# Optimization experiments

Measured on AMD Instinct MI355X. Metric: run time of the kernel, lower is better.

Reference implementation:

```python
import jax, jax.numpy as jnp
import numpy as np

N_NODES = 100000
N_EDGES = 1600000
IN_DIM, HID_DIM, OUT_DIM = 128, 64, 64


def setup_inputs() -> dict:
    key = jax.random.key(0)
    ks = jax.random.split(key, 8)
    x = jax.random.normal(ks[0], (N_NODES, IN_DIM), dtype=jnp.float32)
    edge_index = jax.random.randint(ks[1], (2, N_EDGES), 0, N_NODES, dtype=jnp.int32)
    edge_weight = jax.random.uniform(ks[2], (N_EDGES,), dtype=jnp.float32)
    # GCNConv parameters (glorot-ish init)
    w1 = jax.random.normal(ks[3], (IN_DIM, HID_DIM), dtype=jnp.float32) / np.sqrt(IN_DIM)
    b1 = jnp.zeros((HID_DIM,), dtype=jnp.float32)
    w2 = jax.random.normal(ks[4], (HID_DIM, OUT_DIM), dtype=jnp.float32) / np.sqrt(HID_DIM)
    b2 = jnp.zeros((OUT_DIM,), dtype=jnp.float32)
    return {"x": x, "edge_index": edge_index, "edge_weight": edge_weight,
            "w1": w1, "b1": b1, "w2": w2, "b2": b2}


def _gcn_conv(h, src, dst, edge_weight, w, b, n_nodes):
    # GCNConv(normalize=False): linear transform, then edge-weighted scatter-add
    # (source_to_target flow: gather from src, scatter-sum into dst), then bias.
    h = h @ w                                   # [N, out]
    msg = h[src] * edge_weight[:, None]          # [E, out] irregular gather
    agg = jax.ops.segment_sum(msg, dst, num_segments=n_nodes)  # [N, out]
    return agg + b


def reference(x, edge_index, edge_weight, w1, b1, w2, b2):
    src, dst = edge_index[0], edge_index[1]
    n = x.shape[0]
    # Dropout is identity in eval mode (training=False).
    h = _gcn_conv(x, src, dst, edge_weight, w1, b1, n)
    h = jax.nn.relu(h)
    out = _gcn_conv(h, src, dst, edge_weight, w2, b2, n)
    return out
```

## Files before the change

kernel.cpp:

```cpp
#include <hip/hip_runtime.h>
#include <hip/hip_bf16.h>


#define N_NODES 100000
#define N_EDGES 1600000
#define NB1     391
#define T1      4096
#define NT1     391
#define CAP1    4706
#define GB1     782

typedef unsigned short ushort_t;
typedef unsigned int uint_t;
typedef __attribute__((ext_vector_type(8))) short bf16x8;
typedef __attribute__((ext_vector_type(4))) float floatx4;
typedef __attribute__((ext_vector_type(8))) ushort_t ushort8v;

static __device__ __forceinline__ float bf2f(ushort_t h) {
    return __uint_as_float(((uint_t)h) << 16);
}
static __device__ __forceinline__ ushort_t f2bf(float f) {
    uint_t u = __float_as_uint(f);
    u = (u + 0x7FFF + ((u >> 16) & 1)) >> 16;
    return (ushort_t)u;
}

__global__ __launch_bounds__(512) void k_init(int* __restrict__ gcursor)
{
    int t = threadIdx.x;
    if (t < NB1) gcursor[t] = t * CAP1;
}

__global__ __launch_bounds__(512) void k_p1g1(
    const int* __restrict__ src, const int* __restrict__ dst,
    const float* __restrict__ ew, int* __restrict__ gcursor,
    int2* __restrict__ recs1, int E,
    const float* __restrict__ X, const float* __restrict__ W,
    ushort_t* __restrict__ Y, int N)
{
    __shared__ __align__(16) char smem[47296];
    const int tid = threadIdx.x;

    if (blockIdx.x < NT1) {
        int* cnt     = (int*)smem;
        int* start   = cnt + NB1;
        int* cursor  = start + NB1;
        int* gb      = cursor + NB1;
        int* wsum    = (int*)(smem + 6256);
        int* wexc    = wsum + 8;
        int2* stg    = (int2*)(smem + 6336);
        ushort_t* sb = (ushort_t*)(smem + 39104);
        const int t = tid, b = blockIdx.x;
        const int lane = t & 63, wv = t >> 6;

        if (t < NB1) cnt[t] = 0;
        __syncthreads();
        const int e0 = b * T1;
        const int e1 = min(E, e0 + T1);
        for (int e = e0 + t; e < e1; e += 512)
            atomicAdd(&cnt[dst[e] >> 8], 1);
        __syncthreads();

        const int v = (t < NB1) ? cnt[t] : 0;
        int x = v;
        #pragma unroll
        for (int off = 1; off < 64; off <<= 1) {
            int y = __shfl_up(x, off);
            if (lane >= off) x += y;
        }
        if (lane == 63) wsum[wv] = x;
        __syncthreads();
        if (t < 8) {
            int w  = wsum[t];
            int xx = w;
            #pragma unroll
            for (int off = 1; off < 8; off <<= 1) {
                int y = __shfl_up(xx, off);
                if (t >= off) xx += y;
            }
            wexc[t] = xx - w;
        }
        __syncthreads();
        if (t < NB1) {
            int st = x + wexc[wv] - v;
            start[t]  = st;
            cursor[t] = st;
            gb[t]     = atomicAdd(&gcursor[t], v);
        }
        __syncthreads();

        for (int e = e0 + t; e < e1; e += 512) {
            int d  = dst[e];
            int bk = d >> 8;
            int p  = atomicAdd(&cursor[bk], 1);
            int2 r;
            r.x = ((d & 255) << 17) | src[e];
            r.y = __float_as_int(ew[e]);
            stg[p] = r;
            sb[p]  = (ushort_t)bk;
        }
        __syncthreads();
        const int n = e1 - e0;
        for (int i = t; i < n; i += 512) {
            int bk = sb[i];
            recs1[gb[bk] + (i - start[bk])] = stg[i];
        }
    } else {
        ushort_t* sA = (ushort_t*)smem;
        ushort_t* sB = (ushort_t*)(smem + 18432);
        const int b    = blockIdx.x - NT1;
        const int row0 = b * 128;

        for (int i = tid; i < 128 * 16; i += 512) {
            int k = i >> 4, n4 = (i & 15) * 4;
            float4 v = *(const float4*)(W + (size_t)k * 64 + n4);
            sB[(n4 + 0) * 136 + k] = f2bf(v.x);
            sB[(n4 + 1) * 136 + k] = f2bf(v.y);
            sB[(n4 + 2) * 136 + k] = f2bf(v.z);
            sB[(n4 + 3) * 136 + k] = f2bf(v.w);
        }
        for (int i = tid; i < 128 * 16; i += 512) {
            int r = i >> 4, c4 = (i & 15) * 4;
            int rg = row0 + r; if (rg > N - 1) rg = N - 1;
            float4 v = *(const float4*)(X + (size_t)rg * 128 + c4);
            *(ushort4*)(sA + r * 72 + c4) =
                make_ushort4(f2bf(v.x), f2bf(v.y), f2bf(v.z), f2bf(v.w));
        }
        __syncthreads();

        const int wid = tid >> 6, lane = tid & 63;
        const int m = lane & 15, quad = lane >> 4;
        floatx4 acc[4] = {};

        #pragma unroll
        for (int ksl = 0; ksl < 2; ++ksl) {
            bf16x8 a = *(const bf16x8*)(sA + (wid * 16 + m) * 72 + ksl * 32 + quad * 8);
            #pragma unroll
            for (int nt = 0; nt < 4; ++nt) {
                bf16x8 bfr = *(const bf16x8*)(sB + (nt * 16 + m) * 136 + ksl * 32 + quad * 8);
                acc[nt] = __builtin_amdgcn_mfma_f32_16x16x32_bf16(a, bfr, acc[nt], 0, 0, 0);
            }
        }
        __syncthreads();
        for (int i = tid; i < 128 * 16; i += 512) {
            int r = i >> 4, c4 = (i & 15) * 4;
            int rg = row0 + r; if (rg > N - 1) rg = N - 1;
            float4 v = *(const float4*)(X + (size_t)rg * 128 + 64 + c4);
            *(ushort4*)(sA + r * 72 + c4) =
                make_ushort4(f2bf(v.x), f2bf(v.y), f2bf(v.z), f2bf(v.w));
        }
        __syncthreads();
        #pragma unroll
        for (int ksl = 0; ksl < 2; ++ksl) {
            bf16x8 a = *(const bf16x8*)(sA + (wid * 16 + m) * 72 + ksl * 32 + quad * 8);
            #pragma unroll
            for (int nt = 0; nt < 4; ++nt) {
                bf16x8 bfr = *(const bf16x8*)(sB + (nt * 16 + m) * 136 + 64 + ksl * 32 + quad * 8);
                acc[nt] = __builtin_amdgcn_mfma_f32_16x16x32_bf16(a, bfr, acc[nt], 0, 0, 0);
            }
        }
        __syncthreads();
        #pragma unroll
        for (int nt = 0; nt < 4; ++nt)
            #pragma unroll
            for (int r = 0; r < 4; ++r)
                sA[(wid * 16 + quad * 4 + r) * 72 + nt * 16 + m] = f2bf(acc[nt][r]);
        __syncthreads();
        for (int i = tid; i < 128 * 8; i += 512) {
            int rr = i >> 3, c8 = (i & 7) * 8;
            int rg = row0 + rr;
            if (rg < N)
                *(ushort8v*)(Y + (size_t)rg * 64 + c8) =
                    *(const ushort8v*)(sA + rr * 72 + c8);
        }
    }
}

__global__ __launch_bounds__(1024) void k_pass2(
    const int2* __restrict__ recs1, const int* __restrict__ gcursor,
    int2* __restrict__ recs2, int2* __restrict__ nodeinfo, int N)
{
    __shared__ int cnt[256];
    __shared__ int s[256];
    __shared__ int cursor[256];
    const int t = threadIdx.x, b = blockIdx.x;
    const int lo = b * CAP1;
    const int hi = gcursor[b];

    if (t < 256) cnt[t] = 0;
    __syncthreads();
    for (int j = lo + t; j < hi; j += 1024)
        atomicAdd(&cnt[((uint_t)recs1[j].x) >> 17], 1);
    __syncthreads();
    const int v = (t < 256) ? cnt[t] : 0;
    if (t < 256) s[t] = v;
    #pragma unroll
    for (int off = 1; off < 256; off <<= 1) {
        __syncthreads();
        int a = (t >= off && t < 256) ? s[t - off] : 0;
        __syncthreads();
        if (t < 256) s[t] += a;
    }
    __syncthreads();
    if (t < 256) {
        const int stl = s[t] - v;
        cursor[t] = stl;
        const int ng = b * 256 + t;
        if (ng < N) {
            int2 ni; ni.x = lo + stl; ni.y = v;
            nodeinfo[ng] = ni;
        }
    }
    __syncthreads();
    for (int j = lo + t; j < hi; j += 1024) {
        int2 r = recs1[j];
        int dl = ((uint_t)r.x) >> 17;
        int p  = atomicAdd(&cursor[dl], 1);
        int2 o;
        o.x = r.x & 0x1FFFF;
        o.y = r.y;
        recs2[lo + p] = o;
    }
}

__global__ __launch_bounds__(256) void k_gather1(
    const ushort_t* __restrict__ H, const int2* __restrict__ recs,
    const int2* __restrict__ nodeinfo, const float* __restrict__ bias,
    ushort_t* __restrict__ out)
{
    const int wid  = threadIdx.x >> 6;
    const int lane = threadIdx.x & 63;
    const int n0   = (blockIdx.x * 4 + wid) * 2;
    const int n1   = n0 + 1;

    const int2 niA = nodeinfo[n0];
    const int2 niB = nodeinfo[n1];
    int baseA = niA.x; const int endA = niA.x + niA.y;
    int baseB = niB.x; const int endB = niB.x + niB.y;

    const int g  = lane >> 4;
    const int c4 = (lane & 15) * 4;

    float a0 = 0.f, a1 = 0.f, a2 = 0.f, a3 = 0.f;
    float b0 = 0.f, b1 = 0.f, b2 = 0.f, b3 = 0.f;

    while (baseA < endA || baseB < endB) {
        int mA = endA - baseA; if (mA > 64) mA = 64;
        int mB = endB - baseB; if (mB > 64) mB = 64;
        int2 rA = (mA > 0) ? recs[baseA + (lane < mA ? lane : mA - 1)]
                           : make_int2(0, 0);
        int2 rB = (mB > 0) ? recs[baseB + (lane < mB ? lane : mB - 1)]
                           : make_int2(0, 0);
        float wAf = __int_as_float(rA.y);
        float wBf = __int_as_float(rB.y);
        int mm = mA > mB ? mA : mB;
        #pragma unroll 4
        for (int jj = 0; jj < mm; jj += 4) {
            int idx = jj + g;
            int   sA = __shfl(rA.x, idx);
            float wA = __shfl(wAf, idx);
            int   sB = __shfl(rB.x, idx);
            float wB = __shfl(wBf, idx);
            if (idx >= mA) wA = 0.f;
            if (idx >= mB) wB = 0.f;
            ushort4 hA = *(const ushort4*)(H + (size_t)sA * 64 + c4);
            ushort4 hB = *(const ushort4*)(H + (size_t)sB * 64 + c4);
            a0 = fmaf(wA, bf2f(hA.x), a0);
            a1 = fmaf(wA, bf2f(hA.y), a1);
            a2 = fmaf(wA, bf2f(hA.z), a2);
            a3 = fmaf(wA, bf2f(hA.w), a3);
            b0 = fmaf(wB, bf2f(hB.x), b0);
            b1 = fmaf(wB, bf2f(hB.y), b1);
            b2 = fmaf(wB, bf2f(hB.z), b2);
            b3 = fmaf(wB, bf2f(hB.w), b3);
        }
        baseA += 64;
        baseB += 64;
    }
    a0 += __shfl_down(a0, 32); a1 += __shfl_down(a1, 32);
    a2 += __shfl_down(a2, 32); a3 += __shfl_down(a3, 32);
    b0 += __shfl_down(b0, 32); b1 += __shfl_down(b1, 32);
    b2 += __shfl_down(b2, 32); b3 += __shfl_down(b3, 32);
    a0 += __shfl_down(a0, 16); a1 += __shfl_down(a1, 16);
    a2 += __shfl_down(a2, 16); a3 += __shfl_down(a3, 16);
    b0 += __shfl_down(b0, 16); b1 += __shfl_down(b1, 16);
    b2 += __shfl_down(b2, 16); b3 += __shfl_down(b3, 16);

    if (lane < 16) {
        float4 bv = *(const float4*)(bias + c4);
        float vA0 = fmaxf(a0 + bv.x, 0.f), vA1 = fmaxf(a1 + bv.y, 0.f);
        float vA2 = fmaxf(a2 + bv.z, 0.f), vA3 = fmaxf(a3 + bv.w, 0.f);
        float vB0 = fmaxf(b0 + bv.x, 0.f), vB1 = fmaxf(b1 + bv.y, 0.f);
        float vB2 = fmaxf(b2 + bv.z, 0.f), vB3 = fmaxf(b3 + bv.w, 0.f);
        *(ushort4*)(out + (size_t)n0 * 64 + c4) =
            make_ushort4(f2bf(vA0), f2bf(vA1), f2bf(vA2), f2bf(vA3));
        *(ushort4*)(out + (size_t)n1 * 64 + c4) =
            make_ushort4(f2bf(vB0), f2bf(vB1), f2bf(vB2), f2bf(vB3));
    }
}

__global__ __launch_bounds__(256) void k_gather2mm(
    const ushort_t* __restrict__ H, const int2* __restrict__ recs,
    const int2* __restrict__ nodeinfo, const float* __restrict__ bias2,
    const float* __restrict__ W2, float* __restrict__ out)
{
    __shared__ ushort_t sW[64 * 72];
    __shared__ ushort_t strip[4][128];

    const int tid  = threadIdx.x;
    const int wid  = tid >> 6;
    const int lane = tid & 63;
    const int n0   = (blockIdx.x * 4 + wid) * 2;
    const int n1   = n0 + 1;

    for (int i = tid; i < 64 * 16; i += 256) {
        int k = i >> 4, n4 = (i & 15) * 4;
        float4 v = *(const float4*)(W2 + (size_t)k * 64 + n4);
        sW[(n4 + 0) * 72 + k] = f2bf(v.x);
        sW[(n4 + 1) * 72 + k] = f2bf(v.y);
        sW[(n4 + 2) * 72 + k] = f2bf(v.z);
        sW[(n4 + 3) * 72 + k] = f2bf(v.w);
    }
    __syncthreads();

    const int2 niA = nodeinfo[n0];
    const int2 niB = nodeinfo[n1];
    int baseA = niA.x; const int endA = niA.x + niA.y;
    int baseB = niB.x; const int endB = niB.x + niB.y;

    const int g  = lane >> 4;
    const int c4 = (lane & 15) * 4;

    float a0 = 0.f, a1 = 0.f, a2 = 0.f, a3 = 0.f;
    float b0 = 0.f, b1 = 0.f, b2 = 0.f, b3 = 0.f;

    while (baseA < endA || baseB < endB) {
        int mA = endA - baseA; if (mA > 64) mA = 64;
        int mB = endB - baseB; if (mB > 64) mB = 64;
        int2 rA = (mA > 0) ? recs[baseA + (lane < mA ? lane : mA - 1)]
                           : make_int2(0, 0);
        int2 rB = (mB > 0) ? recs[baseB + (lane < mB ? lane : mB - 1)]
                           : make_int2(0, 0);
        float wAf = __int_as_float(rA.y);
        float wBf = __int_as_float(rB.y);
        int mm = mA > mB ? mA : mB;
        #pragma unroll 4
        for (int jj = 0; jj < mm; jj += 4) {
            int idx = jj + g;
            int   sA_ = __shfl(rA.x, idx);
            float wA  = __shfl(wAf, idx);
            int   sB_ = __shfl(rB.x, idx);
            float wB  = __shfl(wBf, idx);
            if (idx >= mA) wA = 0.f;
            if (idx >= mB) wB = 0.f;
            ushort4 hA = *(const ushort4*)(H + (size_t)sA_ * 64 + c4);
            ushort4 hB = *(const ushort4*)(H + (size_t)sB_ * 64 + c4);
            a0 = fmaf(wA, bf2f(hA.x), a0);
            a1 = fmaf(wA, bf2f(hA.y), a1);
            a2 = fmaf(wA, bf2f(hA.z), a2);
            a3 = fmaf(wA, bf2f(hA.w), a3);
            b0 = fmaf(wB, bf2f(hB.x), b0);
            b1 = fmaf(wB, bf2f(hB.y), b1);
            b2 = fmaf(wB, bf2f(hB.z), b2);
            b3 = fmaf(wB, bf2f(hB.w), b3);
        }
        baseA += 64;
        baseB += 64;
    }
    a0 += __shfl_down(a0, 32); a1 += __shfl_down(a1, 32);
    a2 += __shfl_down(a2, 32); a3 += __shfl_down(a3, 32);
    b0 += __shfl_down(b0, 32); b1 += __shfl_down(b1, 32);
    b2 += __shfl_down(b2, 32); b3 += __shfl_down(b3, 32);
    a0 += __shfl_down(a0, 16); a1 += __shfl_down(a1, 16);
    a2 += __shfl_down(a2, 16); a3 += __shfl_down(a3, 16);
    b0 += __shfl_down(b0, 16); b1 += __shfl_down(b1, 16);
    b2 += __shfl_down(b2, 16); b3 += __shfl_down(b3, 16);

    if (lane < 16) {
        *(ushort4*)(&strip[wid][0 * 64 + c4]) =
            make_ushort4(f2bf(a0), f2bf(a1), f2bf(a2), f2bf(a3));
        *(ushort4*)(&strip[wid][1 * 64 + c4]) =
            make_ushort4(f2bf(b0), f2bf(b1), f2bf(b2), f2bf(b3));
    }
    __builtin_amdgcn_wave_barrier();

    const int m = lane & 15, quad = lane >> 4;
    const ushort_t* sp = strip[wid];
    floatx4 acc2[4] = {};
    #pragma unroll
    for (int ks = 0; ks < 2; ++ks) {
        bf16x8 a = *(const bf16x8*)(sp + (m & 1) * 64 + ks * 32 + quad * 8);
        #pragma unroll
        for (int nt = 0; nt < 4; ++nt) {
            bf16x8 bfr = *(const bf16x8*)(sW + (nt * 16 + m) * 72 + ks * 32 + quad * 8);
            acc2[nt] = __builtin_amdgcn_mfma_f32_16x16x32_bf16(a, bfr, acc2[nt], 0, 0, 0);
        }
    }
    if (quad == 0) {
        #pragma unroll
        for (int nt = 0; nt < 4; ++nt) {
            float bb0 = bias2[nt * 16 + m];
            out[(size_t)n0 * 64 + nt * 16 + m] = acc2[nt][0] + bb0;
            out[(size_t)n1 * 64 + nt * 16 + m] = acc2[nt][1] + bb0;
        }
    }
}

extern "C" void kernel_launch(void* const* d_in, const int* in_sizes, int n_in,
                              void* d_out, int out_size, void* d_ws, size_t ws_size,
                              hipStream_t stream) {
    const float* x   = (const float*)d_in[0];
    const int*   ei  = (const int*)  d_in[1];
    const float* ew  = (const float*)d_in[2];
    const float* w1  = (const float*)d_in[3];
    const float* b1  = (const float*)d_in[4];
    const float* w2  = (const float*)d_in[5];
    const float* b2  = (const float*)d_in[6];
    float* out = (float*)d_out;

    const int N = N_NODES, E = N_EDGES;
    const int* src = ei;
    const int* dst = ei + E;

    char* p = (char*)d_ws;
    ushort_t* bufA   = (ushort_t*)p;  p += (size_t)N_NODES * 64 * 2;
    int2*     recs2  = (int2*)p;      p += (size_t)NB1 * CAP1 * 8;
    int2*     recs1  = (int2*)p;
    ushort_t* bufB   = (ushort_t*)p;  p += (size_t)NB1 * CAP1 * 8;
    int*      gcur   = (int*)p;       p += 2048;
    int2*     ninfo  = (int2*)p;      p += (size_t)N_NODES * 8;

    k_init <<<1, 512, 0, stream>>>(gcur);
    k_p1g1 <<<NT1 + GB1, 512, 0, stream>>>(src, dst, ew, gcur, recs1, E,
                                           x, w1, bufA, N);
    k_pass2<<<NB1, 1024, 0, stream>>>(recs1, gcur, recs2, ninfo, N);

    k_gather1<<<N / 8, 256, 0, stream>>>(bufA, recs2, ninfo, b1, bufB);

    k_gather2mm<<<N / 8, 256, 0, stream>>>(bufB, recs2, ninfo, b2, w2, out);
}
```

Measured before the change: 245.3 us.

## Load full X tile once, simplify block scan, vectorize output stores

The GEMM branch now stages the whole 128x128 X tile in shared memory at once and runs a single 4-step K loop, instead of two half-K passes separated by barriers. The warp-shuffle two-level prefix scan becomes a shared-memory Hillis-Steele scan with many block barriers. The final output stores of the second gather kernel go through a small shared strip so each lane writes a float4 rather than scalar floats. Shared memory per block grows, which may reduce occupancy, and the new scan adds barrier overhead.

```diff
diff --git a/kernel.cpp b/kernel.cpp
--- a/kernel.cpp
+++ b/kernel.cpp
@@ -38,7 +38,7 @@
     const float* __restrict__ X, const float* __restrict__ W,
     ushort_t* __restrict__ Y, int N)
 {
-    __shared__ __align__(16) char smem[47296];
+    __shared__ __align__(16) char smem[52224];
     const int tid = threadIdx.x;
 
     if (blockIdx.x < NT1) {
@@ -46,12 +46,10 @@
         int* start   = cnt + NB1;
         int* cursor  = start + NB1;
         int* gb      = cursor + NB1;
-        int* wsum    = (int*)(smem + 6256);
-        int* wexc    = wsum + 8;
-        int2* stg    = (int2*)(smem + 6336);
-        ushort_t* sb = (ushort_t*)(smem + 39104);
+        int* s       = (int*)(smem + 6256);
+        int2* stg    = (int2*)(smem + 8304);
+        ushort_t* sb = (ushort_t*)(smem + 41072);
         const int t = tid, b = blockIdx.x;
-        const int lane = t & 63, wv = t >> 6;
 
         if (t < NB1) cnt[t] = 0;
         __syncthreads();
@@ -60,35 +58,23 @@
         for (int e = e0 + t; e < e1; e += 512)
             atomicAdd(&cnt[dst[e] >> 8], 1);
         __syncthreads();
-
         const int v = (t < NB1) ? cnt[t] : 0;
-        int x = v;
+        s[t] = v;
         #pragma unroll
-        for (int off = 1; off < 64; off <<= 1) {
-            int y = __shfl_up(x, off);
-            if (lane >= off) x += y;
-        }
-        if (lane == 63) wsum[wv] = x;
-        __syncthreads();
-        if (t < 8) {
-            int w  = wsum[t];
-            int xx = w;
-            #pragma unroll
-            for (int off = 1; off < 8; off <<= 1) {
-                int y = __shfl_up(xx, off);
-                if (t >= off) xx += y;
-            }
-            wexc[t] = xx - w;
+        for (int off = 1; off < 512; off <<= 1) {
+            __syncthreads();
+            int a = (t >= off) ? s[t - off] : 0;
+            __syncthreads();
+            s[t] += a;
         }
         __syncthreads();
         if (t < NB1) {
-            int st = x + wexc[wv] - v;
+            int st = s[t] - v;
             start[t]  = st;
             cursor[t] = st;
             gb[t]     = atomicAdd(&gcursor[t], v);
         }
         __syncthreads();
-
         for (int e = e0 + t; e < e1; e += 512) {
             int d  = dst[e];
             int bk = d >> 8;
@@ -107,10 +93,17 @@
         }
     } else {
         ushort_t* sA = (ushort_t*)smem;
-        ushort_t* sB = (ushort_t*)(smem + 18432);
+        ushort_t* sB = (ushort_t*)(smem + 34816);
         const int b    = blockIdx.x - NT1;
         const int row0 = b * 128;
 
+        for (int i = tid; i < 128 * 32; i += 512) {
+            int r = i >> 5, c4 = (i & 31) * 4;
+            int rg = row0 + r; if (rg > N - 1) rg = N - 1;
+            float4 v = *(const float4*)(X + (size_t)rg * 128 + c4);
+            ushort4 pk = make_ushort4(f2bf(v.x), f2bf(v.y), f2bf(v.z), f2bf(v.w));
+            *(ushort4*)(sA + r * 136 + c4) = pk;
+        }
         for (int i = tid; i < 128 * 16; i += 512) {
             int k = i >> 4, n4 = (i & 15) * 4;
             float4 v = *(const float4*)(W + (size_t)k * 64 + n4);
@@ -119,13 +112,6 @@
             sB[(n4 + 2) * 136 + k] = f2bf(v.z);
             sB[(n4 + 3) * 136 + k] = f2bf(v.w);
         }
-        for (int i = tid; i < 128 * 16; i += 512) {
-            int r = i >> 4, c4 = (i & 15) * 4;
-            int rg = row0 + r; if (rg > N - 1) rg = N - 1;
-            float4 v = *(const float4*)(X + (size_t)rg * 128 + c4);
-            *(ushort4*)(sA + r * 72 + c4) =
-                make_ushort4(f2bf(v.x), f2bf(v.y), f2bf(v.z), f2bf(v.w));
-        }
         __syncthreads();
 
         const int wid = tid >> 6, lane = tid & 63;
@@ -133,29 +119,11 @@
         floatx4 acc[4] = {};
 
         #pragma unroll
-        for (int ksl = 0; ksl < 2; ++ksl) {
-            bf16x8 a = *(const bf16x8*)(sA + (wid * 16 + m) * 72 + ksl * 32 + quad * 8);
+        for (int ks = 0; ks < 4; ++ks) {
+            bf16x8 a = *(const bf16x8*)(sA + (wid * 16 + m) * 136 + ks * 32 + quad * 8);
             #pragma unroll
             for (int nt = 0; nt < 4; ++nt) {
-                bf16x8 bfr = *(const bf16x8*)(sB + (nt * 16 + m) * 136 + ksl * 32 + quad * 8);
-                acc[nt] = __builtin_amdgcn_mfma_f32_16x16x32_bf16(a, bfr, acc[nt], 0, 0, 0);
-            }
-        }
-        __syncthreads();
-        for (int i = tid; i < 128 * 16; i += 512) {
-            int r = i >> 4, c4 = (i & 15) * 4;
-            int rg = row0 + r; if (rg > N - 1) rg = N - 1;
-            float4 v = *(const float4*)(X + (size_t)rg * 128 + 64 + c4);
-            *(ushort4*)(sA + r * 72 + c4) =
-                make_ushort4(f2bf(v.x), f2bf(v.y), f2bf(v.z), f2bf(v.w));
-        }
-        __syncthreads();
-        #pragma unroll
-        for (int ksl = 0; ksl < 2; ++ksl) {
-            bf16x8 a = *(const bf16x8*)(sA + (wid * 16 + m) * 72 + ksl * 32 + quad * 8);
-            #pragma unroll
-            for (int nt = 0; nt < 4; ++nt) {
-                bf16x8 bfr = *(const bf16x8*)(sB + (nt * 16 + m) * 136 + 64 + ksl * 32 + quad * 8);
+                bf16x8 bfr = *(const bf16x8*)(sB + (nt * 16 + m) * 136 + ks * 32 + quad * 8);
                 acc[nt] = __builtin_amdgcn_mfma_f32_16x16x32_bf16(a, bfr, acc[nt], 0, 0, 0);
             }
         }
@@ -306,6 +274,7 @@
 {
     __shared__ ushort_t sW[64 * 72];
     __shared__ ushort_t strip[4][128];
+    __shared__ float    fstrip[4][128];
 
     const int tid  = threadIdx.x;
     const int wid  = tid >> 6;
@@ -399,10 +368,19 @@
     if (quad == 0) {
         #pragma unroll
         for (int nt = 0; nt < 4; ++nt) {
-            float bb0 = bias2[nt * 16 + m];
-            out[(size_t)n0 * 64 + nt * 16 + m] = acc2[nt][0] + bb0;
-            out[(size_t)n1 * 64 + nt * 16 + m] = acc2[nt][1] + bb0;
-        }
+            fstrip[wid][0 * 64 + nt * 16 + m] = acc2[nt][0];
+            fstrip[wid][1 * 64 + nt * 16 + m] = acc2[nt][1];
+        }
+    }
+    __builtin_amdgcn_wave_barrier();
+
+    if (lane < 32) {
+        int rr  = lane >> 4;
+        int mm2 = (lane & 15) * 4;
+        float4 v  = *(const float4*)(&fstrip[wid][rr * 64 + mm2]);
+        float4 bv = *(const float4*)(bias2 + mm2);
+        *(float4*)(out + (size_t)(n0 + rr) * 64 + mm2) =
+            make_float4(v.x + bv.x, v.y + bv.y, v.z + bv.z, v.w + bv.w);
     }
 }
 
```

After: 243.2 us. No clear change (-0.8%).
